# Performance work log

Measured on AMD Instinct MI355X. Metric: run time of the kernel, lower is better.

The kernel has to match this reference:

```python
import jax, jax.numpy as jnp
import numpy as np

B, T, M = 8, 512, 80
U = 896          # RNN_Size (even)
C = 256          # Class


def setup_inputs() -> dict:
    key = jax.random.key(0)
    ks = jax.random.split(key, 13)
    s = 0.05
    d = {
        'mels': jax.random.normal(ks[0], (B, T, M), jnp.float32),
        'Wk':  jax.random.normal(ks[1], (M + 3, 3 * U), jnp.float32) * s,
        'Wr':  jax.random.normal(ks[2], (U, 3 * U), jnp.float32) * s,
        'b':   jax.random.normal(ks[3], (2, 3 * U), jnp.float32) * s,
        'W1c': jax.random.normal(ks[4], (U // 2, U // 2), jnp.float32) * s,
        'b1c': jax.random.normal(ks[5], (U // 2,), jnp.float32) * s,
        'W2c': jax.random.normal(ks[6], (U // 2, C), jnp.float32) * s,
        'b2c': jax.random.normal(ks[7], (C,), jnp.float32) * s,
        'W1f': jax.random.normal(ks[8], (U // 2, U // 2), jnp.float32) * s,
        'b1f': jax.random.normal(ks[9], (U // 2,), jnp.float32) * s,
        'W2f': jax.random.normal(ks[10], (U // 2, C), jnp.float32) * s,
        'b2f': jax.random.normal(ks[11], (C,), jnp.float32) * s,
    }
    return d


def reference(mels, Wk, Wr, b, W1c, b1c, W2c, b2c, W1f, b1f, W2f, b2f):
    # Keras GRUCell (reset_after=True) step.
    def gru(x, h):
        mx = x @ Wk + b[0]                     # [B, 3U]
        mi = h @ Wr + b[1]                     # [B, 3U]
        xz, xr, xh = jnp.split(mx, 3, axis=-1)
        iz, ir, ih = jnp.split(mi, 3, axis=-1)
        z = jax.nn.sigmoid(xz + iz)
        r = jax.nn.sigmoid(xr + ir)
        hh = jnp.tanh(xh + r * ih)
        return z * h + (1.0 - z) * hh

    def head(h, W1, b1, W2, b2):
        return jax.nn.relu(h @ W1 + b1) @ W2 + b2

    Bv = mels.shape[0]
    Tv = mels.shape[1]
    keys = jax.random.split(jax.random.key(42), Tv)
    mels_t = jnp.swapaxes(mels, 0, 1)          # [T, B, M]

    def step(carry, xs):
        coarse, fine, hidden = carry           # [B,1],[B,1],[B,U]
        mel, key = xs
        kc, kf = jax.random.split(key)
        dummy = jnp.zeros_like(coarse)
        # coarse pass (hidden NOT updated, faithful to original)
        x0 = jnp.concatenate([mel, coarse, fine, dummy], axis=-1)
        h0 = gru(x0, hidden)
        logit_c = head(h0[:, :U // 2], W1c, b1c, W2c, b2c)
        # original feeds softmax probs into tf.random.categorical (which
        # expects logits) -- reproduce that faithfully.
        probs_c = jax.nn.softmax(logit_c, axis=-1)
        new_c = jax.random.categorical(kc, probs_c, axis=-1).astype(mels.dtype)[:, None]
        new_c_val = new_c / 255.0 * 2.0 - 1.0
        # fine pass (hidden IS updated)
        x1 = jnp.concatenate([mel, coarse, fine, new_c_val], axis=-1)
        h1 = gru(x1, hidden)
        logit_f = head(h1[:, U // 2:], W1f, b1f, W2f, b2f)
        probs_f = jax.nn.softmax(logit_f, axis=-1)
        new_f = jax.random.categorical(kf, probs_f, axis=-1).astype(mels.dtype)[:, None]
        new_f_val = new_f / 255.0 * 2.0 - 1.0
        sample = (new_c * C + new_f) / 32767.5 - 1.0   # [B,1]
        return (new_c_val, new_f_val, h1), sample[:, 0]

    init = (jnp.zeros((Bv, 1), mels.dtype),
            jnp.zeros((Bv, 1), mels.dtype),
            jnp.zeros((Bv, U), mels.dtype))
    _, samples = jax.lax.scan(step, init, (mels_t, keys))
    return jnp.swapaxes(samples, 0, 1)         # [B, T]
```

## Files before the change

### kernel.cpp

```cpp
#include <hip/hip_runtime.h>
#include <cstdint>
#include <math.h>

#define U 896
#define HU 448
#define TU 2688
#define TT 512
#define MM 80
#define CC 256
#define NTH 512
#define NBLK 72

__device__ __forceinline__ uint32_t rotl32(uint32_t v, int r){ return (v<<r)|(v>>(32-r)); }

__device__ void threefry(uint32_t k0, uint32_t k1, uint32_t x0, uint32_t x1,
                         uint32_t* o0, uint32_t* o1){
  uint32_t k2 = k0 ^ k1 ^ 0x1BD11BDAu;
  x0 += k0; x1 += k1;
  x0+=x1; x1=rotl32(x1,13); x1^=x0;
  x0+=x1; x1=rotl32(x1,15); x1^=x0;
  x0+=x1; x1=rotl32(x1,26); x1^=x0;
  x0+=x1; x1=rotl32(x1, 6); x1^=x0;
  x0+=k1; x1+=k2+1u;
  x0+=x1; x1=rotl32(x1,17); x1^=x0;
  x0+=x1; x1=rotl32(x1,29); x1^=x0;
  x0+=x1; x1=rotl32(x1,16); x1^=x0;
  x0+=x1; x1=rotl32(x1,24); x1^=x0;
  x0+=k2; x1+=k0+2u;
  x0+=x1; x1=rotl32(x1,13); x1^=x0;
  x0+=x1; x1=rotl32(x1,15); x1^=x0;
  x0+=x1; x1=rotl32(x1,26); x1^=x0;
  x0+=x1; x1=rotl32(x1, 6); x1^=x0;
  x0+=k0; x1+=k1+3u;
  x0+=x1; x1=rotl32(x1,17); x1^=x0;
  x0+=x1; x1=rotl32(x1,29); x1^=x0;
  x0+=x1; x1=rotl32(x1,16); x1^=x0;
  x0+=x1; x1=rotl32(x1,24); x1^=x0;
  x0+=k1; x1+=k2+4u;
  x0+=x1; x1=rotl32(x1,13); x1^=x0;
  x0+=x1; x1=rotl32(x1,15); x1^=x0;
  x0+=x1; x1=rotl32(x1,26); x1^=x0;
  x0+=x1; x1=rotl32(x1, 6); x1^=x0;
  x0+=k2; x1+=k0+5u;
  *o0 = x0; *o1 = x1;
}

__device__ float gumbel_from(uint32_t ka, uint32_t kb, uint32_t e){
  uint32_t o0, o1;
  threefry(ka, kb, 0u, e, &o0, &o1);
  uint32_t bits = o0 ^ o1;
  uint32_t m = bits >> 9;
  float u = (m == 0u) ? 1.17549435e-38f
                      : (__uint_as_float(m | 0x3f800000u) - 1.0f);
  float l1 = (float)log((double)u);
  float l2 = (float)log((double)(-l1));
  return -l2;
}

__device__ __forceinline__ float sig_f(float x){
  return (float)(0.5 + 0.5*tanh(0.5*(double)x));
}
__device__ __forceinline__ float tanh_f(float x){ return (float)tanh((double)x); }

__device__ __forceinline__ float gldf(const float* p){
  return __hip_atomic_load(p, __ATOMIC_RELAXED, __HIP_MEMORY_SCOPE_AGENT);
}
__device__ __forceinline__ void gstf(float* p, float v){
  __hip_atomic_store(p, v, __ATOMIC_RELAXED, __HIP_MEMORY_SCOPE_AGENT);
}
__device__ __forceinline__ int gldi(const int* p){
  return __hip_atomic_load(p, __ATOMIC_RELAXED, __HIP_MEMORY_SCOPE_AGENT);
}
__device__ __forceinline__ void gsti(int* p, int v){
  __hip_atomic_store(p, v, __ATOMIC_RELAXED, __HIP_MEMORY_SCOPE_AGENT);
}
__device__ __forceinline__ float2 gldf2(const float* p){
  unsigned long long v = __hip_atomic_load((const unsigned long long*)p,
                                           __ATOMIC_RELAXED, __HIP_MEMORY_SCOPE_AGENT);
  union { unsigned long long u; float2 f; } cv; cv.u = v; return cv.f;
}
__device__ __forceinline__ void gstf2(float* p, float2 f){
  union { float2 f; unsigned long long u; } cv; cv.f = f;
  __hip_atomic_store((unsigned long long*)p, cv.u,
                     __ATOMIC_RELAXED, __HIP_MEMORY_SCOPE_AGENT);
}

__device__ __forceinline__ void wait_slots(const uint32_t* slots, int n, uint32_t tgt, int tid){
  if (tid < n){
    const uint32_t* p = slots + (size_t)tid*32;
    int it = 0;
    while (__hip_atomic_load(p, __ATOMIC_RELAXED, __HIP_MEMORY_SCOPE_AGENT) < tgt){
      __builtin_amdgcn_s_sleep(1);
      if (++it > (1<<22)) break;
    }
  }
  __syncthreads();
}
__device__ __forceinline__ void wait_slots2(const uint32_t* s0, int n0,
                                            const uint32_t* s1, int n1,
                                            uint32_t tgt, int tid){
  const uint32_t* p = nullptr;
  if (tid < n0) p = s0 + (size_t)tid*32;
  else if (tid >= 32 && tid < 32 + n1) p = s1 + (size_t)(tid-32)*32;
  if (p){
    int it = 0;
    while (__hip_atomic_load(p, __ATOMIC_RELAXED, __HIP_MEMORY_SCOPE_AGENT) < tgt){
      __builtin_amdgcn_s_sleep(1);
      if (++it > (1<<22)) break;
    }
  }
  __syncthreads();
}
__device__ __forceinline__ void publish_slot(uint32_t* slot, uint32_t v, int tid){
  __syncthreads();
  if (tid == 0)
    __hip_atomic_store(slot, v, __ATOMIC_RELEASE, __HIP_MEMORY_SCOPE_AGENT);
}

__device__ __forceinline__ void fma4(float4& a, const float4& w, float h){
  a.x += w.x*h; a.y += w.y*h; a.z += w.z*h; a.w += w.w*h;
}

__device__ __forceinline__ void bf8(float4* a){
  #pragma unroll
  for (int d=8; d<64; d<<=1){
    #pragma unroll
    for (int b=0;b<8;++b){
      a[b].x += __shfl_xor(a[b].x, d);
      a[b].y += __shfl_xor(a[b].y, d);
      a[b].z += __shfl_xor(a[b].z, d);
      a[b].w += __shfl_xor(a[b].w, d);
    }
  }
}

__device__ __forceinline__ int sample256(float l0, float l1, float l2, float l3,
                                         const float g[4], int gl){
  float m = fmaxf(fmaxf(l0,l1), fmaxf(l2,l3));
  #pragma unroll
  for (int d=1; d<64; d<<=1) m = fmaxf(m, __shfl_xor(m, d));
  const float e0 = (float)exp((double)(l0-m));
  const float e1 = (float)exp((double)(l1-m));
  const float e2 = (float)exp((double)(l2-m));
  const float e3 = (float)exp((double)(l3-m));
  float ss = ((e0+e1)+(e2+e3));
  #pragma unroll
  for (int d=1; d<64; d<<=1) ss += __shfl_xor(ss, d);
  const float v0 = e0/ss + g[0], v1 = e1/ss + g[1];
  const float v2 = e2/ss + g[2], v3 = e3/ss + g[3];
  float v = v0; int bi = 4*gl;
  if (v1 > v){ v = v1; bi = 4*gl+1; }
  float vB = v2; int biB = 4*gl+2;
  if (v3 > vB){ vB = v3; biB = 4*gl+3; }
  if (vB > v || (vB == v && biB < bi)){ v = vB; bi = biB; }
  #pragma unroll
  for (int d=1; d<64; d<<=1){
    const float ov = __shfl_xor(v, d);
    const int   oi = __shfl_xor(bi, d);
    if (ov > v || (ov == v && oi < bi)){ v = ov; bi = oi; }
  }
  return bi;
}

__global__ __launch_bounds__(256) void k_keys(uint32_t* __restrict__ kc, uint32_t* __restrict__ kf){
  int t = blockIdx.x*256 + threadIdx.x;
  if (t >= TT) return;
  uint32_t ka, kb;
  threefry(0u, 42u, 0u, (uint32_t)t, &ka, &kb);
  uint32_t c0,c1,f0,f1;
  threefry(ka, kb, 0u, 0u, &c0, &c1);
  threefry(ka, kb, 0u, 1u, &f0, &f1);
  kc[2*t] = c0; kc[2*t+1] = c1;
  kf[2*t] = f0; kf[2*t+1] = f1;
}

#define O_SH1   0
#define O_SH1HI 1024
#define O_SFV   2048
#define O_SG    3072
#define O_SYC   6656
#define O_SYF   10240
#define O_KC    13824
#define O_KF    17920
#define O_NCV   22016
#define O_FVS   22080
#define O_NCI   22144
#define O_PRE   22272
#define O_IHB   108288
#define O_HGL   136960
#define O_H0C   194304
#define O_PLC   208640
#define O_PLF   438016
#define WS_ZERO 667392

__global__ __launch_bounds__(NTH, 2) void wavernn_persist(
    const float* __restrict__ mels, const float* __restrict__ Wk,
    const float* __restrict__ Wr,  const float* __restrict__ bias,
    const float* __restrict__ W1c, const float* __restrict__ b1c,
    const float* __restrict__ W2c, const float* __restrict__ b2c,
    const float* __restrict__ W1f, const float* __restrict__ b1f,
    const float* __restrict__ W2f, const float* __restrict__ b2f,
    float* __restrict__ out, char* __restrict__ ws)
{
  uint32_t* SH1   = (uint32_t*)(ws + O_SH1);
  uint32_t* SH1HI = (uint32_t*)(ws + O_SH1HI);
  uint32_t* SFV   = (uint32_t*)(ws + O_SFV);
  uint32_t* SG    = (uint32_t*)(ws + O_SG);
  uint32_t* SYC   = (uint32_t*)(ws + O_SYC);
  uint32_t* SYF   = (uint32_t*)(ws + O_SYF);
  const uint32_t* kc = (const uint32_t*)(ws + O_KC);
  const uint32_t* kf = (const uint32_t*)(ws + O_KF);
  float* ncvB = (float*)(ws + O_NCV);
  float* fvsB = (float*)(ws + O_FVS);
  int*   nci  = (int*)  (ws + O_NCI);
  float* pre  = (float*)(ws + O_PRE);
  float* ihb  = (float*)(ws + O_IHB);
  float* hgl  = (float*)(ws + O_HGL);
  float* h0c  = (float*)(ws + O_H0C);
  float* plgtC= (float*)(ws + O_PLC);
  float* plgtF= (float*)(ws + O_PLF);

  __shared__ __align__(16) char smem[46080];
  const int bk = blockIdx.x, tid = threadIdx.x;

  if (bk < 28){
    const int ks = tid >> 3, k0 = ks*14;
    const int lane = tid & 63, wv = tid >> 6;
    const int U0 = bk*32;
    const int cb0 = U0 + (tid & 7)*4;
    float* hlf   = (float*)smem;
    float* wredf = (float*)(smem + 32768);
    float* gbuf  = (float*)(smem + 41984);
    const int xk = 896 + ks*2;
    const int r0 = ((xk   < 978) ? xk   : 978) - 896;
    const int r1 = ((xk+1 < 978) ? xk+1 : 978) - 896;

    for (int t=0; t<TT; ++t){
      wait_slots(SH1, 8, (uint32_t)t, tid);
      {
        float2 hv[7];
        #pragma unroll
        for (int q=0;q<7;++q) hv[q] = gldf2(hgl + (t&1)*7168 + ((tid + q*NTH)/448)*896 + ((tid + q*NTH) - ((tid + q*NTH)/448)*448)*2);
        #pragma unroll
        for (int q=0;q<7;++q){
          const int i = tid + q*NTH, b = i/448, kp = (i - b*448)*2;
          hlf[b*1024 + kp] = hv[q].x; hlf[b*1024 + kp + 1] = hv[q].y;
        }
      }
      #pragma unroll
      for (int q=0;q<2;++q){
        const int i = tid + q*NTH, b = i>>7, k2 = i&127;
        float v = 0.f;
        if (k2 < 80) v = mels[((size_t)b*TT + t)*MM + k2];
        else if (k2 == 80) v = gldf(ncvB + ((t+1)&1)*8 + b);
        hlf[b*1024 + 896 + k2] = v;
      }
      __syncthreads();

      for (int g=0; g<3; ++g){
        const int cbg = g*896 + cb0;
        float4 aW[8], aX[8];
        #pragma unroll
        for (int b=0;b<8;++b){ aW[b]=make_float4(0,0,0,0); aX[b]=make_float4(0,0,0,0); }
        #pragma unroll 2
        for (int jj=0;jj<14;++jj){
          const float4 w = *(const float4*)(Wr + (size_t)(k0+jj)*TU + cbg);
          #pragma unroll
          for (int b=0;b<8;++b) fma4(aW[b], w, hlf[b*1024 + k0 + jj]);
        }
        {
          const float4 w0 = *(const float4*)(Wk + (size_t)r0*TU + cbg);
          const float4 w1 = *(const float4*)(Wk + (size_t)r1*TU + cbg);
          #pragma unroll
          for (int b=0;b<8;++b){
            fma4(aX[b], w0, hlf[b*1024 + 896 + ks*2]);
            fma4(aX[b], w1, hlf[b*1024 + 897 + ks*2]);
          }
        }
        if (g < 2){
          #pragma unroll
          for (int b=0;b<8;++b){
            aW[b].x += aX[b].x; aW[b].y += aX[b].y;
            aW[b].z += aX[b].z; aW[b].w += aX[b].w;
          }
          bf8(aW);
          if (lane < 8){
            float* dst = wredf + wv*288 + lane*36;
            #pragma unroll
            for (int b=0;b<8;++b) *(float4*)(dst + b*4) = aW[b];
          }
          __syncthreads();
          if (tid < 128){
            const int rb = tid>>4, rq = tid&15;
            float s0 = 0.f, s1 = 0.f;
            #pragma unroll
            for (int w=0; w<8; ++w){
              const float* wp = wredf + w*288 + (rq>>1)*36 + rb*4 + ((2*rq)&3);
              s0 += wp[0]; s1 += wp[1];
            }
            const int col0 = g*896 + U0 + 2*rq;
            const float v0 = s0 + bias[col0]   + bias[TU + col0];
            const float v1 = s1 + bias[col0+1] + bias[TU + col0+1];
            gstf2(pre + rb*TU + col0, make_float2(v0, v1));
            gbuf[(rb*32 + 2*rq)*4 + g] = v0;
            gbuf[(rb*32 + 2*rq + 1)*4 + g] = v1;
          }
          __syncthreads();
        } else {
          bf8(aW);
          if (lane < 8){
            float* dst = wredf + wv*288 + lane*36;
            #pragma unroll
            for (int b=0;b<8;++b) *(float4*)(dst + b*4) = aW[b];
          }
          __syncthreads();
          if (tid < 128){
            const int rb = tid>>4, rq = tid&15;
            float s0 = 0.f, s1 = 0.f;
            #pragma unroll
            for (int w=0; w<8; ++w){
              const float* wp = wredf + w*288 + (rq>>1)*36 + rb*4 + ((2*rq)&3);
              s0 += wp[0]; s1 += wp[1];
            }
            const int u0 = U0 + 2*rq;
            const float v0 = s0 + bias[TU + 1792 + u0];
            const float v1 = s1 + bias[TU + 1792 + u0 + 1];
            gstf2(ihb + rb*896 + u0, make_float2(v0, v1));
            gbuf[(rb*32 + 2*rq)*4 + 3] = v0;
            gbuf[(rb*32 + 2*rq + 1)*4 + 3] = v1;
          }
          __syncthreads();
          bf8(aX);
          if (lane < 8){
            float* dst = wredf + wv*288 + lane*36;
            #pragma unroll
            for (int b=0;b<8;++b) *(float4*)(dst + b*4) = aX[b];
          }
          __syncthreads();
          if (tid < 128){
            const int rb = tid>>4, rq = tid&15;
            float s0 = 0.f, s1 = 0.f;
            #pragma unroll
            for (int w=0; w<8; ++w){
              const float* wp = wredf + w*288 + (rq>>1)*36 + rb*4 + ((2*rq)&3);
              s0 += wp[0]; s1 += wp[1];
            }
            const int u0 = U0 + 2*rq;
            const float v0 = s0 + bias[1792 + u0];
            const float v1 = s1 + bias[1792 + u0 + 1];
            gstf2(pre + rb*TU + 1792 + u0, make_float2(v0, v1));
            gbuf[(rb*32 + 2*rq)*4 + 2] = v0;
            gbuf[(rb*32 + 2*rq + 1)*4 + 2] = v1;
          }
          __syncthreads();
        }
      }

      if (bk < 14){
        wait_slots(SFV, 8, (uint32_t)t, tid);
        if (tid < 128){
          const int b = tid>>4, q = tid&15;
          const int u0 = U0 + 2*q;
          const float fv = gldf(fvsB + ((t+1)&1)*8 + b);
          const float2 wz = *(const float2*)(Wk + (size_t)81*TU + u0);
          const float2 wr = *(const float2*)(Wk + (size_t)81*TU + 896 + u0);
          const float2 wx = *(const float2*)(Wk + (size_t)81*TU + 1792 + u0);
          const float* g0 = gbuf + (b*32 + 2*q)*4;
          const float* g1 = g0 + 4;
          const float az0 = g0[0] + fv*wz.x, az1 = g1[0] + fv*wz.y;
          const float ar0 = g0[1] + fv*wr.x, ar1 = g1[1] + fv*wr.y;
          const float ax0 = g0[2] + fv*wx.x, ax1 = g1[2] + fv*wx.y;
          const float z0 = sig_f(az0), z1 = sig_f(az1);
          const float r0g = sig_f(ar0), r1g = sig_f(ar1);
          const float hh0 = tanh_f(ax0 + r0g*g0[3]);
          const float hh1 = tanh_f(ax1 + r1g*g1[3]);
          const float o0 = z0*hlf[b*1024 + u0]     + (1.0f - z0)*hh0;
          const float o1 = z1*hlf[b*1024 + u0 + 1] + (1.0f - z1)*hh1;
          gstf2(h0c + b*HU + u0, make_float2(o0, o1));
        }
      }
      publish_slot(SG + bk*32, (uint32_t)(t+1), tid);
    }
  } else if (bk < 56){
    const int j = bk - 28;
    float* hstg = (float*)smem;
    float* red1 = (float*)(smem + 14336);
    float* y1s  = (float*)(smem + 16384);
    const int outp = tid & 127, ks4 = tid >> 7;
    const int ob = outp >> 4, oc = outp & 15;
    const int i0 = ks4*112;

    for (int t=0; t<TT; ++t){
      wait_slots(SG, 14, (uint32_t)(t+1), tid);
      {
        float2 hv[4];
        #pragma unroll
        for (int q=0;q<4;++q){
          const int i = tid + q*NTH;
          if (i < 1792) hv[q] = gldf2(h0c + 2*i);
        }
        #pragma unroll
        for (int q=0;q<4;++q){
          const int i = tid + q*NTH;
          if (i < 1792){ hstg[2*i] = hv[q].x; hstg[2*i+1] = hv[q].y; }
        }
      }
      __syncthreads();
      {
        float s = 0.f;
        const float* hb = hstg + ob*HU;
        const float* wb = W1c + (size_t)i0*HU + j*16 + oc;
        #pragma unroll 4
        for (int i=0;i<112;++i) s += hb[i0+i]*wb[(size_t)i*HU];
        red1[outp*4 + ks4] = s;
      }
      __syncthreads();
      if (tid < 128){
        const float v = (red1[tid*4+0]+red1[tid*4+1])+(red1[tid*4+2]+red1[tid*4+3]);
        y1s[tid] = fmaxf(v + b1c[j*16 + (tid&15)], 0.0f);
      }
      __syncthreads();
      #pragma unroll
      for (int p=0;p<2;++p){
        const int po = p*512 + tid;
        const int b = po>>7, cc0 = (po&127)*2;
        float sa = 0.f, sb = 0.f;
        #pragma unroll
        for (int i=0;i<16;++i){
          const float yv = y1s[b*16+i];
          const float2 w2 = *(const float2*)(W2c + (size_t)(j*16+i)*CC + cc0);
          sa += yv*w2.x; sb += yv*w2.y;
        }
        gstf2(plgtC + j*2048 + b*256 + cc0, make_float2(sa, sb));
      }
      publish_slot(SYC + j*32, (uint32_t)(t+1), tid);

      wait_slots(SH1HI, 8, (uint32_t)(t+1), tid);
      const int hsN = ((t+1)&1)*7168;
      {
        float2 hv[4];
        #pragma unroll
        for (int q=0;q<4;++q){
          const int i = tid + q*NTH;
          if (i < 1792){
            const int b = i/224, ii0 = (i - b*224)*2;
            hv[q] = gldf2(hgl + hsN + b*896 + 448 + ii0);
          }
        }
        #pragma unroll
        for (int q=0;q<4;++q){
          const int i = tid + q*NTH;
          if (i < 1792){
            const int b = i/224, ii0 = (i - b*224)*2;
            hstg[b*448 + ii0] = hv[q].x; hstg[b*448 + ii0 + 1] = hv[q].y;
          }
        }
      }
      __syncthreads();
      {
        float s = 0.f;
        const float* hb = hstg + ob*HU;
        const float* wb = W1f + (size_t)i0*HU + j*16 + oc;
        #pragma unroll 4
        for (int i=0;i<112;++i) s += hb[i0+i]*wb[(size_t)i*HU];
        red1[outp*4 + ks4] = s;
      }
      __syncthreads();
      if (tid < 128){
        const float v = (red1[tid*4+0]+red1[tid*4+1])+(red1[tid*4+2]+red1[tid*4+3]);
        y1s[tid] = fmaxf(v + b1f[j*16 + (tid&15)], 0.0f);
      }
      __syncthreads();
      #pragma unroll
      for (int p=0;p<2;++p){
        const int po = p*512 + tid;
        const int b = po>>7, cc0 = (po&127)*2;
        float sa = 0.f, sb = 0.f;
        #pragma unroll
        for (int i=0;i<16;++i){
          const float yv = y1s[b*16+i];
          const float2 w2 = *(const float2*)(W2f + (size_t)(j*16+i)*CC + cc0);
          sa += yv*w2.x; sb += yv*w2.y;
        }
        gstf2(plgtF + j*2048 + b*256 + cc0, make_float2(sa, sb));
      }
      publish_slot(SYF + j*32, (uint32_t)(t+1), tid);
    }
  } else if (bk < 64){
    const int b = bk - 56;
    __shared__ int ncSh;
    for (int t=0; t<TT; ++t){
      float gc[4];
      if (tid < 64){
        const uint32_t ka = kc[2*t], kb2 = kc[2*t+1];
        #pragma unroll
        for (int i=0;i<4;++i)
          gc[i] = gumbel_from(ka, kb2, (uint32_t)(b*CC + 4*tid + i));
      }
      wait_slots2(SYC, 28, SG, 28, (uint32_t)(t+1), tid);
      if (tid < 64){
        float s0=0.f,s1=0.f,s2=0.f,s3=0.f;
        const float* pb = plgtC + b*256 + 4*tid;
        #pragma unroll
        for (int h=0; h<2; ++h){
          float2 pA[14], pB[14];
          #pragma unroll
          for (int q=0;q<14;++q){
            pA[q] = gldf2(pb + (h*14+q)*2048);
            pB[q] = gldf2(pb + (h*14+q)*2048 + 2);
          }
          #pragma unroll
          for (int q=0;q<14;++q){
            s0 += pA[q].x; s1 += pA[q].y; s2 += pB[q].x; s3 += pB[q].y;
          }
        }
        const float l0 = s0 + b2c[4*tid+0], l1 = s1 + b2c[4*tid+1];
        const float l2 = s2 + b2c[4*tid+2], l3 = s3 + b2c[4*tid+3];
        const int nc = sample256(l0,l1,l2,l3, gc, tid);
        if (tid == 0){
          gsti(nci + b, nc);
          gstf(ncvB + (t&1)*8 + b, (float)nc/255.0f*2.0f - 1.0f);
          ncSh = nc;
        }
      }
      __syncthreads();
      const float ncv = (float)ncSh/255.0f*2.0f - 1.0f;
      const float fv = gldf(fvsB + ((t+1)&1)*8 + b);
      const int hsO = (t&1)*7168, hsN = ((t+1)&1)*7168;
      if (tid < 224){
        const int u0 = 448 + 2*tid;
        const float2 pz = gldf2(pre + b*TU + u0);
        const float2 pr = gldf2(pre + b*TU + 896 + u0);
        const float2 px = gldf2(pre + b*TU + 1792 + u0);
        const float2 ih = gldf2(ihb + b*896 + u0);
        const float2 ho = gldf2(hgl + hsO + b*896 + u0);
        const float2 w81z = *(const float2*)(Wk + (size_t)81*TU + u0);
        const float2 w81r = *(const float2*)(Wk + (size_t)81*TU + 896 + u0);
        const float2 w81x = *(const float2*)(Wk + (size_t)81*TU + 1792 + u0);
        const float2 w82z = *(const float2*)(Wk + (size_t)82*TU + u0);
        const float2 w82r = *(const float2*)(Wk + (size_t)82*TU + 896 + u0);
        const float2 w82x = *(const float2*)(Wk + (size_t)82*TU + 1792 + u0);
        const float az0 = pz.x + fv*w81z.x + ncv*w82z.x;
        const float az1 = pz.y + fv*w81z.y + ncv*w82z.y;
        const float ar0 = pr.x + fv*w81r.x + ncv*w82r.x;
        const float ar1 = pr.y + fv*w81r.y + ncv*w82r.y;
        const float ax0 = px.x + fv*w81x.x + ncv*w82x.x;
        const float ax1 = px.y + fv*w81x.y + ncv*w82x.y;
        const float z0 = sig_f(az0), z1 = sig_f(az1);
        const float r0g = sig_f(ar0), r1g = sig_f(ar1);
        const float h0v = z0*ho.x + (1.0f - z0)*tanh_f(ax0 + r0g*ih.x);
        const float h1v = z1*ho.y + (1.0f - z1)*tanh_f(ax1 + r1g*ih.y);
        gstf2(hgl + hsN + b*896 + u0, make_float2(h0v, h1v));
      }
      publish_slot(SH1HI + b*32, (uint32_t)(t+1), tid);
      if (tid < 224){
        const int u0 = 2*tid;
        const float2 pz = gldf2(pre + b*TU + u0);
        const float2 pr = gldf2(pre + b*TU + 896 + u0);
        const float2 px = gldf2(pre + b*TU + 1792 + u0);
        const float2 ih = gldf2(ihb + b*896 + u0);
        const float2 ho = gldf2(hgl + hsO + b*896 + u0);
        const float2 w81z = *(const float2*)(Wk + (size_t)81*TU + u0);
        const float2 w81r = *(const float2*)(Wk + (size_t)81*TU + 896 + u0);
        const float2 w81x = *(const float2*)(Wk + (size_t)81*TU + 1792 + u0);
        const float2 w82z = *(const float2*)(Wk + (size_t)82*TU + u0);
        const float2 w82r = *(const float2*)(Wk + (size_t)82*TU + 896 + u0);
        const float2 w82x = *(const float2*)(Wk + (size_t)82*TU + 1792 + u0);
        const float az0 = pz.x + fv*w81z.x + ncv*w82z.x;
        const float az1 = pz.y + fv*w81z.y + ncv*w82z.y;
        const float ar0 = pr.x + fv*w81r.x + ncv*w82r.x;
        const float ar1 = pr.y + fv*w81r.y + ncv*w82r.y;
        const float ax0 = px.x + fv*w81x.x + ncv*w82x.x;
        const float ax1 = px.y + fv*w81x.y + ncv*w82x.y;
        const float z0 = sig_f(az0), z1 = sig_f(az1);
        const float r0g = sig_f(ar0), r1g = sig_f(ar1);
        const float h0v = z0*ho.x + (1.0f - z0)*tanh_f(ax0 + r0g*ih.x);
        const float h1v = z1*ho.y + (1.0f - z1)*tanh_f(ax1 + r1g*ih.y);
        gstf2(hgl + hsN + b*896 + u0, make_float2(h0v, h1v));
      }
      publish_slot(SH1 + b*32, (uint32_t)(t+1), tid);
    }
  } else {
    const int b = bk - 64;
    for (int t=0; t<TT; ++t){
      float gf[4];
      if (tid < 64){
        const uint32_t ka = kf[2*t], kb2 = kf[2*t+1];
        #pragma unroll
        for (int i=0;i<4;++i)
          gf[i] = gumbel_from(ka, kb2, (uint32_t)(b*CC + 4*tid + i));
      }
      wait_slots(SYF, 28, (uint32_t)(t+1), tid);
      if (tid < 64){
        float s0=0.f,s1=0.f,s2=0.f,s3=0.f;
        const float* pb = plgtF + b*256 + 4*tid;
        #pragma unroll
        for (int h=0; h<2; ++h){
          float2 pA[14], pB[14];
          #pragma unroll
          for (int q=0;q<14;++q){
            pA[q] = gldf2(pb + (h*14+q)*2048);
            pB[q] = gldf2(pb + (h*14+q)*2048 + 2);
          }
          #pragma unroll
          for (int q=0;q<14;++q){
            s0 += pA[q].x; s1 += pA[q].y; s2 += pB[q].x; s3 += pB[q].y;
          }
        }
        const float l0 = s0 + b2f[4*tid+0], l1 = s1 + b2f[4*tid+1];
        const float l2 = s2 + b2f[4*tid+2], l3 = s3 + b2f[4*tid+3];
        const int nf = sample256(l0,l1,l2,l3, gf, tid);
        if (tid == 0){
          gstf(fvsB + (t&1)*8 + b, (float)nf/255.0f*2.0f - 1.0f);
          const int nc = gldi(nci + b);
          out[(size_t)b*TT + t] = ((float)nc*256.0f + (float)nf)/32767.5f - 1.0f;
        }
      }
      publish_slot(SFV + b*32, (uint32_t)(t+1), tid);
    }
  }
}

extern "C" void kernel_launch(void* const* d_in, const int* in_sizes, int n_in,
                              void* d_out, int out_size, void* d_ws, size_t ws_size,
                              hipStream_t stream) {
  const float* mels = (const float*)d_in[0];
  const float* Wk   = (const float*)d_in[1];
  const float* Wr   = (const float*)d_in[2];
  const float* bias = (const float*)d_in[3];
  const float* W1c  = (const float*)d_in[4];
  const float* b1c  = (const float*)d_in[5];
  const float* W2c  = (const float*)d_in[6];
  const float* b2c  = (const float*)d_in[7];
  const float* W1f  = (const float*)d_in[8];
  const float* b1f  = (const float*)d_in[9];
  const float* W2f  = (const float*)d_in[10];
  const float* b2f  = (const float*)d_in[11];
  float* out = (float*)d_out;
  char* wsb = (char*)d_ws;

  uint32_t* kc = (uint32_t*)(wsb + O_KC);
  uint32_t* kf = (uint32_t*)(wsb + O_KF);

  hipMemsetAsync(d_ws, 0, WS_ZERO, stream);
  k_keys<<<2,256,0,stream>>>(kc, kf);

  void* args[] = { (void*)&mels, (void*)&Wk, (void*)&Wr, (void*)&bias,
                   (void*)&W1c, (void*)&b1c, (void*)&W2c, (void*)&b2c,
                   (void*)&W1f, (void*)&b1f, (void*)&W2f, (void*)&b2f,
                   (void*)&out, (void*)&wsb };
  hipLaunchCooperativeKernel((const void*)wavernn_persist, dim3(NBLK), dim3(NTH),
                             args, 0, stream);
}
```

Before: 17.81 ms.

## Move coarse-pass GRU gate combine into head blocks, drop h0c round trip

The coarse-pass hidden state h0 is no longer computed by the first 14 GRU blocks and written to a global h0c buffer. Instead, each coarse-head block reads the preactivations (pre, ihb) and the previous hidden state, adds the coarse/fine feedback term itself, and applies the gates straight into shared memory. This takes the SFV wait and the gate math off the critical path of the GRU blocks and removes one inter-block handoff. In exchange, each of the 28 head blocks recomputes the full 8x448 gate combine redundantly and issues more global loads per step. The sampler block now also waits on SFV directly.

```diff
diff --git a/kernel.cpp b/kernel.cpp
--- a/kernel.cpp
+++ b/kernel.cpp
@@ -96,21 +96,6 @@
   }
   __syncthreads();
 }
-__device__ __forceinline__ void wait_slots2(const uint32_t* s0, int n0,
-                                            const uint32_t* s1, int n1,
-                                            uint32_t tgt, int tid){
-  const uint32_t* p = nullptr;
-  if (tid < n0) p = s0 + (size_t)tid*32;
-  else if (tid >= 32 && tid < 32 + n1) p = s1 + (size_t)(tid-32)*32;
-  if (p){
-    int it = 0;
-    while (__hip_atomic_load(p, __ATOMIC_RELAXED, __HIP_MEMORY_SCOPE_AGENT) < tgt){
-      __builtin_amdgcn_s_sleep(1);
-      if (++it > (1<<22)) break;
-    }
-  }
-  __syncthreads();
-}
 __device__ __forceinline__ void publish_slot(uint32_t* slot, uint32_t v, int tid){
   __syncthreads();
   if (tid == 0)
@@ -216,7 +201,6 @@
   float* pre  = (float*)(ws + O_PRE);
   float* ihb  = (float*)(ws + O_IHB);
   float* hgl  = (float*)(ws + O_HGL);
-  float* h0c  = (float*)(ws + O_H0C);
   float* plgtC= (float*)(ws + O_PLC);
   float* plgtF= (float*)(ws + O_PLF);
 
@@ -230,7 +214,6 @@
     const int cb0 = U0 + (tid & 7)*4;
     float* hlf   = (float*)smem;
     float* wredf = (float*)(smem + 32768);
-    float* gbuf  = (float*)(smem + 41984);
     const int xk = 896 + ks*2;
     const int r0 = ((xk   < 978) ? xk   : 978) - 896;
     const int r1 = ((xk+1 < 978) ? xk+1 : 978) - 896;
@@ -302,8 +285,6 @@
             const float v0 = s0 + bias[col0]   + bias[TU + col0];
             const float v1 = s1 + bias[col0+1] + bias[TU + col0+1];
             gstf2(pre + rb*TU + col0, make_float2(v0, v1));
-            gbuf[(rb*32 + 2*rq)*4 + g] = v0;
-            gbuf[(rb*32 + 2*rq + 1)*4 + g] = v1;
           }
           __syncthreads();
         } else {
@@ -323,11 +304,9 @@
               s0 += wp[0]; s1 += wp[1];
             }
             const int u0 = U0 + 2*rq;
-            const float v0 = s0 + bias[TU + 1792 + u0];
-            const float v1 = s1 + bias[TU + 1792 + u0 + 1];
-            gstf2(ihb + rb*896 + u0, make_float2(v0, v1));
-            gbuf[(rb*32 + 2*rq)*4 + 3] = v0;
-            gbuf[(rb*32 + 2*rq + 1)*4 + 3] = v1;
+            gstf2(ihb + rb*896 + u0,
+                  make_float2(s0 + bias[TU + 1792 + u0],
+                              s1 + bias[TU + 1792 + u0 + 1]));
           }
           __syncthreads();
           bf8(aX);
@@ -346,44 +325,18 @@
               s0 += wp[0]; s1 += wp[1];
             }
             const int u0 = U0 + 2*rq;
-            const float v0 = s0 + bias[1792 + u0];
-            const float v1 = s1 + bias[1792 + u0 + 1];
-            gstf2(pre + rb*TU + 1792 + u0, make_float2(v0, v1));
-            gbuf[(rb*32 + 2*rq)*4 + 2] = v0;
-            gbuf[(rb*32 + 2*rq + 1)*4 + 2] = v1;
+            gstf2(pre + rb*TU + 1792 + u0,
+                  make_float2(s0 + bias[1792 + u0],
+                              s1 + bias[1792 + u0 + 1]));
           }
           __syncthreads();
-        }
-      }
-
-      if (bk < 14){
-        wait_slots(SFV, 8, (uint32_t)t, tid);
-        if (tid < 128){
-          const int b = tid>>4, q = tid&15;
-          const int u0 = U0 + 2*q;
-          const float fv = gldf(fvsB + ((t+1)&1)*8 + b);
-          const float2 wz = *(const float2*)(Wk + (size_t)81*TU + u0);
-          const float2 wr = *(const float2*)(Wk + (size_t)81*TU + 896 + u0);
-          const float2 wx = *(const float2*)(Wk + (size_t)81*TU + 1792 + u0);
-          const float* g0 = gbuf + (b*32 + 2*q)*4;
-          const float* g1 = g0 + 4;
-          const float az0 = g0[0] + fv*wz.x, az1 = g1[0] + fv*wz.y;
-          const float ar0 = g0[1] + fv*wr.x, ar1 = g1[1] + fv*wr.y;
-          const float ax0 = g0[2] + fv*wx.x, ax1 = g1[2] + fv*wx.y;
-          const float z0 = sig_f(az0), z1 = sig_f(az1);
-          const float r0g = sig_f(ar0), r1g = sig_f(ar1);
-          const float hh0 = tanh_f(ax0 + r0g*g0[3]);
-          const float hh1 = tanh_f(ax1 + r1g*g1[3]);
-          const float o0 = z0*hlf[b*1024 + u0]     + (1.0f - z0)*hh0;
-          const float o1 = z1*hlf[b*1024 + u0 + 1] + (1.0f - z1)*hh1;
-          gstf2(h0c + b*HU + u0, make_float2(o0, o1));
         }
       }
       publish_slot(SG + bk*32, (uint32_t)(t+1), tid);
     }
   } else if (bk < 56){
     const int j = bk - 28;
-    float* hstg = (float*)smem;
+    float* h0s  = (float*)smem;
     float* red1 = (float*)(smem + 14336);
     float* y1s  = (float*)(smem + 16384);
     const int outp = tid & 127, ks4 = tid >> 7;
@@ -392,23 +345,33 @@
 
     for (int t=0; t<TT; ++t){
       wait_slots(SG, 14, (uint32_t)(t+1), tid);
-      {
-        float2 hv[4];
-        #pragma unroll
-        for (int q=0;q<4;++q){
-          const int i = tid + q*NTH;
-          if (i < 1792) hv[q] = gldf2(h0c + 2*i);
-        }
-        #pragma unroll
-        for (int q=0;q<4;++q){
-          const int i = tid + q*NTH;
-          if (i < 1792){ hstg[2*i] = hv[q].x; hstg[2*i+1] = hv[q].y; }
-        }
+      float azv[7], arv[7], axv[7], ihv[7], hov[7];
+      const int hsLo = (t&1)*7168;
+      #pragma unroll
+      for (int q=0;q<7;++q){
+        const int i = tid + q*NTH, b = i/448, u = i - b*448;
+        azv[q] = gldf(pre + b*TU + u);
+        arv[q] = gldf(pre + b*TU + 896 + u);
+        axv[q] = gldf(pre + b*TU + 1792 + u);
+        ihv[q] = gldf(ihb + b*896 + u);
+        hov[q] = gldf(hgl + hsLo + b*896 + u);
+      }
+      wait_slots(SFV, 8, (uint32_t)t, tid);
+      #pragma unroll
+      for (int q=0;q<7;++q){
+        const int i = tid + q*NTH, b = i/448, u = i - b*448;
+        const float fv = gldf(fvsB + ((t+1)&1)*8 + b);
+        const float az = azv[q] + fv*Wk[(size_t)81*TU + u];
+        const float ar = arv[q] + fv*Wk[(size_t)81*TU + 896 + u];
+        const float ax = axv[q] + fv*Wk[(size_t)81*TU + 1792 + u];
+        const float z = sig_f(az), r = sig_f(ar);
+        const float hh = tanh_f(ax + r*ihv[q]);
+        h0s[i] = z*hov[q] + (1.0f - z)*hh;
       }
       __syncthreads();
       {
         float s = 0.f;
-        const float* hb = hstg + ob*HU;
+        const float* hb = h0s + ob*HU;
         const float* wb = W1c + (size_t)i0*HU + j*16 + oc;
         #pragma unroll 4
         for (int i=0;i<112;++i) s += hb[i0+i]*wb[(size_t)i*HU];
@@ -452,14 +415,14 @@
           const int i = tid + q*NTH;
           if (i < 1792){
             const int b = i/224, ii0 = (i - b*224)*2;
-            hstg[b*448 + ii0] = hv[q].x; hstg[b*448 + ii0 + 1] = hv[q].y;
+            h0s[b*448 + ii0] = hv[q].x; h0s[b*448 + ii0 + 1] = hv[q].y;
           }
         }
       }
       __syncthreads();
       {
         float s = 0.f;
-        const float* hb = hstg + ob*HU;
+        const float* hb = h0s + ob*HU;
         const float* wb = W1f + (size_t)i0*HU + j*16 + oc;
         #pragma unroll 4
         for (int i=0;i<112;++i) s += hb[i0+i]*wb[(size_t)i*HU];
@@ -497,7 +460,20 @@
         for (int i=0;i<4;++i)
           gc[i] = gumbel_from(ka, kb2, (uint32_t)(b*CC + 4*tid + i));
       }
-      wait_slots2(SYC, 28, SG, 28, (uint32_t)(t+1), tid);
+      {
+        const uint32_t* p = nullptr; uint32_t tgt = 0;
+        if (tid < 28){ p = SYC + (size_t)tid*32; tgt = (uint32_t)(t+1); }
+        else if (tid >= 32 && tid < 60){ p = SG + (size_t)(tid-32)*32; tgt = (uint32_t)(t+1); }
+        else if (tid >= 64 && tid < 72){ p = SFV + (size_t)(tid-64)*32; tgt = (uint32_t)t; }
+        if (p){
+          int it = 0;
+          while (__hip_atomic_load(p, __ATOMIC_RELAXED, __HIP_MEMORY_SCOPE_AGENT) < tgt){
+            __builtin_amdgcn_s_sleep(1);
+            if (++it > (1<<22)) break;
+          }
+        }
+        __syncthreads();
+      }
       if (tid < 64){
         float s0=0.f,s1=0.f,s2=0.f,s3=0.f;
         const float* pb = plgtC + b*256 + 4*tid;
```

Result: slower. 24.55 ms (+37.9%).

## Move coarse-pass GRU finalization into per-batch fine-sampler blocks

Applied to the files above, without the earlier changes.

The coarse-pass hidden state h0 used to be computed by the first 14 GRU blocks after they waited on the fine-sample flag. That step now runs in the 8 per-batch fine-sampling blocks, right after they draw the fine sample. They read the full pre-activations from global memory and publish a new SH0C flag that the coarse head blocks wait on. This takes the fine-sample wait off the GRU blocks' critical path and shortens the dependency chain, at the cost of extra global reads of pre, ihb and hgl in the sampler blocks.

```diff
diff --git a/kernel.cpp b/kernel.cpp
--- a/kernel.cpp
+++ b/kernel.cpp
@@ -176,7 +176,7 @@
 
 #define O_SH1   0
 #define O_SH1HI 1024
-#define O_SFV   2048
+#define O_SH0C  2048
 #define O_SG    3072
 #define O_SYC   6656
 #define O_SYF   10240
@@ -204,7 +204,7 @@
 {
   uint32_t* SH1   = (uint32_t*)(ws + O_SH1);
   uint32_t* SH1HI = (uint32_t*)(ws + O_SH1HI);
-  uint32_t* SFV   = (uint32_t*)(ws + O_SFV);
+  uint32_t* SH0C  = (uint32_t*)(ws + O_SH0C);
   uint32_t* SG    = (uint32_t*)(ws + O_SG);
   uint32_t* SYC   = (uint32_t*)(ws + O_SYC);
   uint32_t* SYF   = (uint32_t*)(ws + O_SYF);
@@ -230,7 +230,6 @@
     const int cb0 = U0 + (tid & 7)*4;
     float* hlf   = (float*)smem;
     float* wredf = (float*)(smem + 32768);
-    float* gbuf  = (float*)(smem + 41984);
     const int xk = 896 + ks*2;
     const int r0 = ((xk   < 978) ? xk   : 978) - 896;
     const int r1 = ((xk+1 < 978) ? xk+1 : 978) - 896;
@@ -299,11 +298,9 @@
               s0 += wp[0]; s1 += wp[1];
             }
             const int col0 = g*896 + U0 + 2*rq;
-            const float v0 = s0 + bias[col0]   + bias[TU + col0];
-            const float v1 = s1 + bias[col0+1] + bias[TU + col0+1];
-            gstf2(pre + rb*TU + col0, make_float2(v0, v1));
-            gbuf[(rb*32 + 2*rq)*4 + g] = v0;
-            gbuf[(rb*32 + 2*rq + 1)*4 + g] = v1;
+            gstf2(pre + rb*TU + col0,
+                  make_float2(s0 + bias[col0]   + bias[TU + col0],
+                              s1 + bias[col0+1] + bias[TU + col0+1]));
           }
           __syncthreads();
         } else {
@@ -323,11 +320,9 @@
               s0 += wp[0]; s1 += wp[1];
             }
             const int u0 = U0 + 2*rq;
-            const float v0 = s0 + bias[TU + 1792 + u0];
-            const float v1 = s1 + bias[TU + 1792 + u0 + 1];
-            gstf2(ihb + rb*896 + u0, make_float2(v0, v1));
-            gbuf[(rb*32 + 2*rq)*4 + 3] = v0;
-            gbuf[(rb*32 + 2*rq + 1)*4 + 3] = v1;
+            gstf2(ihb + rb*896 + u0,
+                  make_float2(s0 + bias[TU + 1792 + u0],
+                              s1 + bias[TU + 1792 + u0 + 1]));
           }
           __syncthreads();
           bf8(aX);
@@ -346,37 +341,11 @@
               s0 += wp[0]; s1 += wp[1];
             }
             const int u0 = U0 + 2*rq;
-            const float v0 = s0 + bias[1792 + u0];
-            const float v1 = s1 + bias[1792 + u0 + 1];
-            gstf2(pre + rb*TU + 1792 + u0, make_float2(v0, v1));
-            gbuf[(rb*32 + 2*rq)*4 + 2] = v0;
-            gbuf[(rb*32 + 2*rq + 1)*4 + 2] = v1;
+            gstf2(pre + rb*TU + 1792 + u0,
+                  make_float2(s0 + bias[1792 + u0],
+                              s1 + bias[1792 + u0 + 1]));
           }
           __syncthreads();
-        }
-      }
-
-      if (bk < 14){
-        wait_slots(SFV, 8, (uint32_t)t, tid);
-        if (tid < 128){
-          const int b = tid>>4, q = tid&15;
-          const int u0 = U0 + 2*q;
-          const float fv = gldf(fvsB + ((t+1)&1)*8 + b);
-          const float2 wz = *(const float2*)(Wk + (size_t)81*TU + u0);
-          const float2 wr = *(const float2*)(Wk + (size_t)81*TU + 896 + u0);
-          const float2 wx = *(const float2*)(Wk + (size_t)81*TU + 1792 + u0);
-          const float* g0 = gbuf + (b*32 + 2*q)*4;
-          const float* g1 = g0 + 4;
-          const float az0 = g0[0] + fv*wz.x, az1 = g1[0] + fv*wz.y;
-          const float ar0 = g0[1] + fv*wr.x, ar1 = g1[1] + fv*wr.y;
-          const float ax0 = g0[2] + fv*wx.x, ax1 = g1[2] + fv*wx.y;
-          const float z0 = sig_f(az0), z1 = sig_f(az1);
-          const float r0g = sig_f(ar0), r1g = sig_f(ar1);
-          const float hh0 = tanh_f(ax0 + r0g*g0[3]);
-          const float hh1 = tanh_f(ax1 + r1g*g1[3]);
-          const float o0 = z0*hlf[b*1024 + u0]     + (1.0f - z0)*hh0;
-          const float o1 = z1*hlf[b*1024 + u0 + 1] + (1.0f - z1)*hh1;
-          gstf2(h0c + b*HU + u0, make_float2(o0, o1));
         }
       }
       publish_slot(SG + bk*32, (uint32_t)(t+1), tid);
@@ -391,7 +360,7 @@
     const int i0 = ks4*112;
 
     for (int t=0; t<TT; ++t){
-      wait_slots(SG, 14, (uint32_t)(t+1), tid);
+      wait_slots(SH0C, 8, (uint32_t)(t+1), tid);
       {
         float2 hv[4];
         #pragma unroll
@@ -582,6 +551,23 @@
     }
   } else {
     const int b = bk - 64;
+    __shared__ float fvSh;
+
+    wait_slots(SG, 28, 1u, tid);
+    if (tid < 224){
+      const int u0 = 2*tid;
+      const float2 pz = gldf2(pre + b*TU + u0);
+      const float2 pr = gldf2(pre + b*TU + 896 + u0);
+      const float2 px = gldf2(pre + b*TU + 1792 + u0);
+      const float2 ih = gldf2(ihb + b*896 + u0);
+      const float z0 = sig_f(pz.x), z1 = sig_f(pz.y);
+      const float r0g = sig_f(pr.x), r1g = sig_f(pr.y);
+      const float h0v = (1.0f - z0)*tanh_f(px.x + r0g*ih.x);
+      const float h1v = (1.0f - z1)*tanh_f(px.y + r1g*ih.y);
+      gstf2(h0c + b*HU + u0, make_float2(h0v, h1v));
+    }
+    publish_slot(SH0C + b*32, 1u, tid);
+
     for (int t=0; t<TT; ++t){
       float gf[4];
       if (tid < 64){
@@ -611,12 +597,41 @@
         const float l2 = s2 + b2f[4*tid+2], l3 = s3 + b2f[4*tid+3];
         const int nf = sample256(l0,l1,l2,l3, gf, tid);
         if (tid == 0){
-          gstf(fvsB + (t&1)*8 + b, (float)nf/255.0f*2.0f - 1.0f);
+          const float fvv = (float)nf/255.0f*2.0f - 1.0f;
+          gstf(fvsB + (t&1)*8 + b, fvv);
+          fvSh = fvv;
           const int nc = gldi(nci + b);
           out[(size_t)b*TT + t] = ((float)nc*256.0f + (float)nf)/32767.5f - 1.0f;
         }
       }
-      publish_slot(SFV + b*32, (uint32_t)(t+1), tid);
+      __syncthreads();
+
+      if (t < TT-1){
+        wait_slots(SG, 28, (uint32_t)(t+2), tid);
+        const float fv = fvSh;
+        if (tid < 224){
+          const int u0 = 2*tid;
+          const float2 pz = gldf2(pre + b*TU + u0);
+          const float2 pr = gldf2(pre + b*TU + 896 + u0);
+          const float2 px = gldf2(pre + b*TU + 1792 + u0);
+          const float2 ih = gldf2(ihb + b*896 + u0);
+          const float2 ho = gldf2(hgl + ((t+1)&1)*7168 + b*896 + u0);
+          const float2 wz = *(const float2*)(Wk + (size_t)81*TU + u0);
+          const float2 wr = *(const float2*)(Wk + (size_t)81*TU + 896 + u0);
+          const float2 wx = *(const float2*)(Wk + (size_t)81*TU + 1792 + u0);
+          const float az0 = pz.x + fv*wz.x, az1 = pz.y + fv*wz.y;
+          const float ar0 = pr.x + fv*wr.x, ar1 = pr.y + fv*wr.y;
+          const float ax0 = px.x + fv*wx.x, ax1 = px.y + fv*wx.y;
+          const float z0 = sig_f(az0), z1 = sig_f(az1);
+          const float r0g = sig_f(ar0), r1g = sig_f(ar1);
+          const float hh0 = tanh_f(ax0 + r0g*ih.x);
+          const float hh1 = tanh_f(ax1 + r1g*ih.y);
+          const float h0v = z0*ho.x + (1.0f - z0)*hh0;
+          const float h1v = z1*ho.y + (1.0f - z1)*hh1;
+          gstf2(h0c + b*HU + u0, make_float2(h0v, h1v));
+        }
+        publish_slot(SH0C + b*32, (uint32_t)(t+2), tid);
+      }
     }
   }
 }
```

Result: slower. 18.28 ms (+2.7%).
